# Optimization experiments

Measured on AMD Instinct MI355X. Metric: run time of the kernel, lower is better.

The kernel has to match this reference:

```python
import jax, jax.numpy as jnp
import numpy as np

D, H_DIM, HEADS = 512, 2048, 8

def rmsnorm(x, w):
    eps = jnp.finfo(x.dtype).eps
    return x * jax.lax.rsqrt(jnp.mean(x * x, axis=-1, keepdims=True) + eps) * w

def setup_inputs() -> dict:
    key = jax.random.key(0)
    ks = jax.random.split(key, 16)
    B, N = 2, 2048
    s_d = 1.0 / np.sqrt(D)
    s_h = 1.0 / np.sqrt(H_DIM)
    inp = {
        "x": jax.random.normal(ks[0], (B, N, D), jnp.float32),
        "DA": jax.random.randint(ks[1], (B, 1, N, N), 0, 2, jnp.int32),
        "Wq": jax.random.normal(ks[2], (D, D), jnp.float32) * s_d,
        "bq": jnp.zeros((D,), jnp.float32),
        "Wk": jax.random.normal(ks[3], (D, D), jnp.float32) * s_d,
        "bk": jnp.zeros((D,), jnp.float32),
        "Wv": jax.random.normal(ks[4], (D, D), jnp.float32) * s_d,
        "bv": jnp.zeros((D,), jnp.float32),
        "W1": jax.random.normal(ks[5], (H_DIM, D), jnp.float32) * s_d,
        "b1": jnp.zeros((H_DIM,), jnp.float32),
        "W2": jax.random.normal(ks[6], (H_DIM, D), jnp.float32) * s_d,
        "b2": jnp.zeros((H_DIM,), jnp.float32),
        "W3": jax.random.normal(ks[7], (D, H_DIM), jnp.float32) * s_h,
        "b3": jnp.zeros((D,), jnp.float32),
        "g1": jnp.ones((D,), jnp.float32),
        "g2": jnp.ones((D,), jnp.float32),
    }
    return inp

def reference(x, DA, Wq, bq, Wk, bk, Wv, bv, W1, b1, W2, b2, W3, b3, g1, g2):
    B, N, _ = x.shape
    hd = D // HEADS  # head_dim = 64
    xn = rmsnorm(x, g1)
    # projections (torch Linear: y = x @ W.T + b), split heads -> [B,H,N,hd]
    def split(t):
        return t.reshape(B, N, HEADS, hd).transpose(0, 2, 1, 3)
    q = split(xn @ Wq.T + bq)
    k = split(xn @ Wk.T + bk)
    v = split(xn @ Wv.T + bv)
    scores = jnp.einsum("bhnd,bhmd->bhnm", q, k) / np.sqrt(hd)
    scores = jnp.where(DA == 0, jnp.asarray(-1e20, scores.dtype), scores)
    attn = jax.nn.softmax(scores, axis=-1)
    o = jnp.einsum("bhnm,bhmd->bhnd", attn, v)
    o = o.transpose(0, 2, 1, 3).reshape(B, N, D)
    h = x + o
    hn = rmsnorm(h, g2)
    x2 = hn @ W1.T + b1
    x3 = hn @ W2.T + b2
    out = h + (jax.nn.silu(x2) * x3) @ W3.T + b3
    return out
```

## Files before the change

kernel.cpp:

```cpp
#include <hip/hip_runtime.h>

typedef unsigned short u16;
typedef unsigned int   u32;
typedef unsigned long long u64;

using bf16x8 = __attribute__((ext_vector_type(8))) __bf16;
using f32x4  = __attribute__((ext_vector_type(4))) float;
using us8    = __attribute__((ext_vector_type(8))) u16;
using us4v   = __attribute__((ext_vector_type(4))) u16;

#define NB_TOK   4096
#define DD       512
#define HDIM     2048
#define SEQ      2048
#define EPS_F32  1.1920929e-7f
#define SM_SHIFT2 23.083120654223414f
#define Q_SCALE   0.18033688011112042f

__device__ __forceinline__ u16 f32_to_bf16(float f) {
  u32 u = __float_as_uint(f);
  u += 0x7fffu + ((u >> 16) & 1u);
  return (u16)(u >> 16);
}
__device__ __forceinline__ float bf16_to_f32(u16 h) {
  return __uint_as_float(((u32)h) << 16);
}
__device__ __forceinline__ bf16x8 ld_frag(const u16* p) {
  return __builtin_bit_cast(bf16x8, *(const us8*)p);
}
__device__ __forceinline__ void gload_lds16(const void* g, void* l) {
  __builtin_amdgcn_global_load_lds(
      (__attribute__((address_space(1))) void*)(void*)g,
      (__attribute__((address_space(3))) void*)l, 16, 0, 0);
}

__global__ __launch_bounds__(256) void k_pre(
    const float* __restrict__ wq, const float* __restrict__ wk,
    const float* __restrict__ wv, const float* __restrict__ w1,
    const float* __restrict__ w2, const float* __restrict__ w3,
    const int* __restrict__ da, const float* __restrict__ x,
    const float* __restrict__ g1,
    u16* __restrict__ wqkv, u16* __restrict__ w1b,
    u16* __restrict__ w2b, u16* __restrict__ w3b,
    u64* __restrict__ maskT, u16* __restrict__ xn) {
  int bx = blockIdx.x;
  if (bx < 3840) {
    int e = (bx * 256 + threadIdx.x) * 4;
    const float* src; u16* dst; int off;
    if      (e <  262144) { src = wq; dst = wqkv;          off = e; }
    else if (e <  524288) { src = wk; dst = wqkv + 262144; off = e -  262144; }
    else if (e <  786432) { src = wv; dst = wqkv + 524288; off = e -  524288; }
    else if (e < 1835008) { src = w1; dst = w1b;           off = e -  786432; }
    else if (e < 2883584) { src = w2; dst = w2b;           off = e - 1835008; }
    else                  { src = w3; dst = w3b;           off = e - 2883584; }
    float4 v = *(const float4*)(src + off);
    us4v o;
    o[0] = f32_to_bf16(v.x); o[1] = f32_to_bf16(v.y);
    o[2] = f32_to_bf16(v.z); o[3] = f32_to_bf16(v.w);
    *(us4v*)(dst + off) = o;
  } else if (bx < 4864) {
    int lane = threadIdx.x & 63, wave = threadIdx.x >> 6;
    int row = (bx - 3840) * 4 + wave;
    int b = row >> 11, r = row & 2047;
    const int* src = da + (size_t)row * SEQ;
    #pragma unroll 4
    for (int w = 0; w < 32; ++w) {
      int d = src[w * 64 + lane];
      u64 bal = __ballot(d != 0);
      if (lane == 0) maskT[((size_t)(b * 32 + w)) * SEQ + r] = bal;
    }
  } else {
    int lane = threadIdx.x & 63, wave = threadIdx.x >> 6;
    int row = (bx - 4864) * 4 + wave;
    size_t base = (size_t)row * DD + lane * 8;
    float4 a = *(const float4*)(x + base);
    float4 b = *(const float4*)(x + base + 4);
    float ss = a.x*a.x + a.y*a.y + a.z*a.z + a.w*a.w
             + b.x*b.x + b.y*b.y + b.z*b.z + b.w*b.w;
    #pragma unroll
    for (int m = 1; m < 64; m <<= 1) ss += __shfl_xor(ss, m);
    float sc = rsqrtf(ss * (1.0f / DD) + EPS_F32);
    float4 ga = *(const float4*)(g1 + lane * 8);
    float4 gb = *(const float4*)(g1 + lane * 8 + 4);
    us8 o;
    o[0] = f32_to_bf16(a.x * sc * ga.x); o[1] = f32_to_bf16(a.y * sc * ga.y);
    o[2] = f32_to_bf16(a.z * sc * ga.z); o[3] = f32_to_bf16(a.w * sc * ga.w);
    o[4] = f32_to_bf16(b.x * sc * gb.x); o[5] = f32_to_bf16(b.y * sc * gb.y);
    o[6] = f32_to_bf16(b.z * sc * gb.z); o[7] = f32_to_bf16(b.w * sc * gb.w);
    *(us8*)(xn + base) = o;
  }
}

template <int NB>
__device__ __forceinline__ void gemm32(const u16* __restrict__ A,
                                       const u16* __restrict__ B0,
                                       const u16* __restrict__ B1,
                                       int K, int mblk, int nblk,
                                       int kbeg, int iters,
                                       u16* lA, u16* lB,
                                       f32x4 (*acc)[4][2]) {
  const int lane = threadIdx.x & 63, wave = threadIdx.x >> 6;
  const int l15 = lane & 15, quad = lane >> 4;
  const int wmt = (wave >> 1) * 4, wnt = (wave & 1) * 2;
  constexpr int CPW = 2 + NB;

  auto stage = [&](int buf, int k0) {
    #pragma unroll
    for (int i = 0; i < CPW; ++i) {
      int id = wave * CPW + i;
      if (id < 8) {
        gload_lds16(A + (size_t)(mblk + id * 16 + l15) * K + k0 + quad * 8,
                    lA + buf * 4096 + id * 512);
      } else {
        int id2 = id - 8, bi = id2 >> 2, nt = id2 & 3;
        const u16* B = bi ? B1 : B0;
        gload_lds16(B + (size_t)(nblk + nt * 16 + l15) * K + k0 + quad * 8,
                    lB + bi * 4096 + buf * 2048 + nt * 512);
      }
    }
  };

  stage(0, kbeg);
  __syncthreads();
  for (int it = 0; it < iters; ++it) {
    if (it + 1 < iters) stage((it + 1) & 1, kbeg + (it + 1) * 32);
    int buf = it & 1;
    bf16x8 af[4];
    #pragma unroll
    for (int mt = 0; mt < 4; ++mt)
      af[mt] = ld_frag(lA + buf * 4096 + (wmt + mt) * 512 + lane * 8);
    #pragma unroll
    for (int bi = 0; bi < NB; ++bi)
      #pragma unroll
      for (int nt = 0; nt < 2; ++nt) {
        bf16x8 b = ld_frag(lB + bi * 4096 + buf * 2048 + (wnt + nt) * 512 + lane * 8);
        #pragma unroll
        for (int mt = 0; mt < 4; ++mt)
          acc[bi][mt][nt] = __builtin_amdgcn_mfma_f32_16x16x32_bf16(
              af[mt], b, acc[bi][mt][nt], 0, 0, 0);
      }
    __syncthreads();
  }
}

__global__ __launch_bounds__(256, 4) void k_qkv(const u16* __restrict__ xn,
                                                const u16* __restrict__ wqkv,
                                                const float* __restrict__ bq,
                                                const float* __restrict__ bk,
                                                const float* __restrict__ bv,
                                                u16* __restrict__ qb,
                                                u16* __restrict__ kb,
                                                u16* __restrict__ vt) {
  __shared__ u16 lA[8192], lB[4096];
  int z = blockIdx.z;
  const u16* Bp = wqkv + z * (DD * DD);
  const float* bias = (z == 0) ? bq : ((z == 1) ? bk : bv);
  float scale = (z == 0) ? Q_SCALE : 1.0f;
  int mblk = blockIdx.x * 128, nblk = blockIdx.y * 64;
  f32x4 acc[1][4][2];
  #pragma unroll
  for (int mt = 0; mt < 4; ++mt)
    #pragma unroll
    for (int nt = 0; nt < 2; ++nt) acc[0][mt][nt] = (f32x4)0.0f;
  gemm32<1>(xn, Bp, nullptr, DD, mblk, nblk, 0, 16, lA, lB, acc);
  int lane = threadIdx.x & 63, wave = threadIdx.x >> 6;
  int l15 = lane & 15, quad = lane >> 4;
  int wm = (wave >> 1) * 64, wn = (wave & 1) * 32;
  if (z < 2) {
    u16* out = z ? kb : qb;
    #pragma unroll
    for (int mt = 0; mt < 4; ++mt)
      #pragma unroll
      for (int nt = 0; nt < 2; ++nt) {
        int n = nblk + wn + nt * 16 + l15;
        float bn = bias[n];
        #pragma unroll
        for (int r = 0; r < 4; ++r) {
          int m = mblk + wm + mt * 16 + quad * 4 + r;
          out[(size_t)m * DD + n] = f32_to_bf16((acc[0][mt][nt][r] + bn) * scale);
        }
      }
  } else {
    #pragma unroll
    for (int mt = 0; mt < 4; ++mt)
      #pragma unroll
      for (int nt = 0; nt < 2; ++nt) {
        int n = nblk + wn + nt * 16 + l15;
        float bn = bias[n];
        int m = mblk + wm + mt * 16 + quad * 4;
        int b = m >> 11, tok = m & 2047;
        us4v o;
        #pragma unroll
        for (int r = 0; r < 4; ++r) o[r] = f32_to_bf16(acc[0][mt][nt][r] + bn);
        *(us4v*)(vt + ((size_t)(b * 8 + (n >> 6)) * 64 + (n & 63)) * SEQ + tok) = o;
      }
  }
}

__global__ __launch_bounds__(256) void k_attn(const u16* __restrict__ q,
                                              const u16* __restrict__ k,
                                              const u16* __restrict__ vT,
                                              const u64* __restrict__ maskT,
                                              u16* __restrict__ Opart,
                                              float* __restrict__ lpart) {
  __shared__ u16 lK[8192], lV[8192], lP[4 * 32 * 72];
  int tid = threadIdx.x, lane = tid & 63, wave = tid >> 6;
  int l15 = lane & 15, quad = lane >> 4;
  int bh = blockIdx.y, b = bh >> 3, h = bh & 7;
  int q0 = blockIdx.x * 128;
  int z = blockIdx.z;
  int kvbase = z * 512;
  const u16* kg = k + (size_t)(b * SEQ + kvbase) * DD + h * 64;
  const u16* vg = vT + (size_t)bh * 64 * SEQ + kvbase;
  const u64* mg = maskT + ((size_t)(b * 32 + z * 8)) * SEQ + q0 + wave * 32 + l15;

  #pragma unroll
  for (int i = 0; i < 2; ++i) {
    int c = wave * 2 + i;
    int mt = c >> 1, ks = c & 1;
    gload_lds16(kg + (size_t)(mt * 16 + l15) * DD + ks * 32 + quad * 8, lK + c * 512);
    gload_lds16(vg + (size_t)(mt * 16 + l15) * SEQ + ks * 32 + quad * 8, lV + c * 512);
  }

  const u16* qrow = q + (size_t)(b * SEQ + q0 + wave * 32 + l15) * DD + h * 64;
  bf16x8 qa[2][2];
  #pragma unroll
  for (int nq = 0; nq < 2; ++nq)
    #pragma unroll
    for (int ks = 0; ks < 2; ++ks)
      qa[nq][ks] = ld_frag(qrow + (size_t)nq * 16 * DD + ks * 32 + quad * 8);
  __syncthreads();

  us8 ones_u;
  #pragma unroll
  for (int j = 0; j < 8; ++j) ones_u[j] = 0x3f80;
  const bf16x8 ones = __builtin_bit_cast(bf16x8, ones_u);

  f32x4 oa[2][4], oal[2];
  #pragma unroll
  for (int mq = 0; mq < 2; ++mq) {
    oal[mq] = (f32x4)0.0f;
    #pragma unroll
    for (int dt = 0; dt < 4; ++dt) oa[mq][dt] = (f32x4)0.0f;
  }

  u16* pw = lP + wave * 2304;

  for (int t = 0; t < 8; ++t) {
    const u16* lKc = lK + (t & 1) * 4096;
    const u16* lVc = lV + (t & 1) * 4096;

    u64 mw[2];
    #pragma unroll
    for (int nq = 0; nq < 2; ++nq)
      mw[nq] = mg[(size_t)t * SEQ + nq * 16] >> (quad * 4);

    if (t + 1 < 8) {
      int kv1 = (t + 1) * 64;
      u16* dK = lK + ((t + 1) & 1) * 4096;
      u16* dV = lV + ((t + 1) & 1) * 4096;
      #pragma unroll
      for (int i = 0; i < 2; ++i) {
        int c = wave * 2 + i;
        int mt = c >> 1, ks = c & 1;
        gload_lds16(kg + (size_t)(kv1 + mt * 16 + l15) * DD + ks * 32 + quad * 8, dK + c * 512);
        gload_lds16(vg + (size_t)(mt * 16 + l15) * SEQ + kv1 + ks * 32 + quad * 8, dV + c * 512);
      }
    }

    f32x4 sa[2][4];
    #pragma unroll
    for (int nq = 0; nq < 2; ++nq)
      #pragma unroll
      for (int mt = 0; mt < 4; ++mt) sa[nq][mt] = (f32x4)0.0f;
    #pragma unroll
    for (int ks = 0; ks < 2; ++ks) {
      bf16x8 ka[4];
      #pragma unroll
      for (int mt = 0; mt < 4; ++mt)
        ka[mt] = ld_frag(lKc + mt * 1024 + ks * 512 + lane * 8);
      #pragma unroll
      for (int nq = 0; nq < 2; ++nq)
        #pragma unroll
        for (int mt = 0; mt < 4; ++mt)
          sa[nq][mt] = __builtin_amdgcn_mfma_f32_16x16x32_bf16(
              ka[mt], qa[nq][ks], sa[nq][mt], 0, 0, 0);
    }

    #pragma unroll
    for (int nq = 0; nq < 2; ++nq)
      #pragma unroll
      for (int mt = 0; mt < 4; ++mt) {
        u32 nib = (u32)(mw[nq] >> (mt * 16)) & 0xFu;
        u32 pb[4];
        #pragma unroll
        for (int r = 0; r < 4; ++r) {
          float p = __builtin_amdgcn_exp2f(sa[nq][mt][r] - SM_SHIFT2);
          p = (nib >> r) & 1u ? p : 0.0f;
          pb[r] = __float_as_uint(p);
        }
        u32 lo = __builtin_amdgcn_perm(pb[1], pb[0], 0x07060302u);
        u32 hi = __builtin_amdgcn_perm(pb[3], pb[2], 0x07060302u);
        u64 pk = ((u64)hi << 32) | lo;
        *(u64*)(pw + (nq * 16 + l15) * 72 + mt * 16 + quad * 4) = pk;
      }

    #pragma unroll
    for (int ks = 0; ks < 2; ++ks) {
      bf16x8 pa[2], vb[4];
      #pragma unroll
      for (int mq = 0; mq < 2; ++mq)
        pa[mq] = ld_frag(pw + (mq * 16 + l15) * 72 + ks * 32 + quad * 8);
      #pragma unroll
      for (int dt = 0; dt < 4; ++dt)
        vb[dt] = ld_frag(lVc + dt * 1024 + ks * 512 + lane * 8);
      #pragma unroll
      for (int mq = 0; mq < 2; ++mq) {
        #pragma unroll
        for (int dt = 0; dt < 4; ++dt)
          oa[mq][dt] = __builtin_amdgcn_mfma_f32_16x16x32_bf16(
              pa[mq], vb[dt], oa[mq][dt], 0, 0, 0);
        oal[mq] = __builtin_amdgcn_mfma_f32_16x16x32_bf16(
            pa[mq], ones, oal[mq], 0, 0, 0);
      }
    }

    __syncthreads();
  }

  if (l15 == 0) {
    #pragma unroll
    for (int mq = 0; mq < 2; ++mq)
      #pragma unroll
      for (int r = 0; r < 4; ++r)
        lpart[((size_t)z * 16 + bh) * SEQ + q0 + wave * 32 + mq * 16 + quad * 4 + r] =
            oal[mq][r];
  }

  u16* Og = Opart + (size_t)z * NB_TOK * DD;
  #pragma unroll
  for (int mq = 0; mq < 2; ++mq)
    #pragma unroll
    for (int r = 0; r < 4; ++r) {
      int m = q0 + wave * 32 + mq * 16 + quad * 4 + r;
      u16* dst = Og + (size_t)(b * SEQ + m) * DD + h * 64;
      #pragma unroll
      for (int dt = 0; dt < 4; ++dt)
        dst[dt * 16 + l15] = f32_to_bf16(oa[mq][dt][r]);
    }
}

__global__ __launch_bounds__(256) void k_rms2(const float* __restrict__ x,
                                              const u16* __restrict__ Opart,
                                              const float* __restrict__ lpart,
                                              const float* __restrict__ b3,
                                              const float* __restrict__ g2,
                                              float* __restrict__ outinit,
                                              u16* __restrict__ hn) {
  int lane = threadIdx.x & 63, wave = threadIdx.x >> 6;
  int row = blockIdx.x * 4 + wave;
  int b = row >> 11, tok = row & 2047, hh = lane >> 3;
  size_t base = (size_t)row * DD + lane * 8;
  float lsum = 0.0f;
  #pragma unroll
  for (int z = 0; z < 4; ++z)
    lsum += lpart[((size_t)(z * 16 + b * 8 + hh)) * SEQ + tok];
  float inv = (lsum > 0.0f) ? (1.0f / lsum) : 0.0f;
  float ov[8] = {0,0,0,0,0,0,0,0};
  #pragma unroll
  for (int z = 0; z < 4; ++z) {
    us8 o = *(const us8*)(Opart + (size_t)z * NB_TOK * DD + base);
    #pragma unroll
    for (int j = 0; j < 8; ++j) ov[j] += bf16_to_f32(o[j]);
  }
  float4 a = *(const float4*)(x + base);
  float4 bb = *(const float4*)(x + base + 4);
  float hv[8];
  hv[0] = a.x  + ov[0] * inv; hv[1] = a.y  + ov[1] * inv;
  hv[2] = a.z  + ov[2] * inv; hv[3] = a.w  + ov[3] * inv;
  hv[4] = bb.x + ov[4] * inv; hv[5] = bb.y + ov[5] * inv;
  hv[6] = bb.z + ov[6] * inv; hv[7] = bb.w + ov[7] * inv;
  float ss = 0.0f;
  #pragma unroll
  for (int j = 0; j < 8; ++j) ss += hv[j] * hv[j];
  #pragma unroll
  for (int m = 1; m < 64; m <<= 1) ss += __shfl_xor(ss, m);
  float sc = rsqrtf(ss * (1.0f / DD) + EPS_F32);
  float4 c0 = *(const float4*)(b3 + lane * 8);
  float4 c1 = *(const float4*)(b3 + lane * 8 + 4);
  float4 w0 = {hv[0] + c0.x, hv[1] + c0.y, hv[2] + c0.z, hv[3] + c0.w};
  float4 w1 = {hv[4] + c1.x, hv[5] + c1.y, hv[6] + c1.z, hv[7] + c1.w};
  *(float4*)(outinit + base) = w0;
  *(float4*)(outinit + base + 4) = w1;
  float4 ga = *(const float4*)(g2 + lane * 8);
  float4 gb = *(const float4*)(g2 + lane * 8 + 4);
  us8 hb;
  hb[0] = f32_to_bf16(hv[0] * sc * ga.x); hb[1] = f32_to_bf16(hv[1] * sc * ga.y);
  hb[2] = f32_to_bf16(hv[2] * sc * ga.z); hb[3] = f32_to_bf16(hv[3] * sc * ga.w);
  hb[4] = f32_to_bf16(hv[4] * sc * gb.x); hb[5] = f32_to_bf16(hv[5] * sc * gb.y);
  hb[6] = f32_to_bf16(hv[6] * sc * gb.z); hb[7] = f32_to_bf16(hv[7] * sc * gb.w);
  *(us8*)(hn + base) = hb;
}

__global__ __launch_bounds__(256, 4) void k_ffn12(const u16* __restrict__ hn,
                                                  const u16* __restrict__ w1,
                                                  const u16* __restrict__ w2,
                                                  const float* __restrict__ b1,
                                                  const float* __restrict__ b2,
                                                  u16* __restrict__ g) {
  __shared__ u16 lA[8192], lB[8192];
  int mblk = blockIdx.x * 128, nblk = blockIdx.y * 64;
  f32x4 acc[2][4][2];
  #pragma unroll
  for (int bi = 0; bi < 2; ++bi)
    #pragma unroll
    for (int mt = 0; mt < 4; ++mt)
      #pragma unroll
      for (int nt = 0; nt < 2; ++nt) acc[bi][mt][nt] = (f32x4)0.0f;
  gemm32<2>(hn, w1, w2, DD, mblk, nblk, 0, 16, lA, lB, acc);
  int lane = threadIdx.x & 63, wave = threadIdx.x >> 6;
  int l15 = lane & 15, quad = lane >> 4;
  int wm = (wave >> 1) * 64, wn = (wave & 1) * 32;
  #pragma unroll
  for (int mt = 0; mt < 4; ++mt)
    #pragma unroll
    for (int nt = 0; nt < 2; ++nt) {
      int n = nblk + wn + nt * 16 + l15;
      float bb1 = b1[n], bb2 = b2[n];
      #pragma unroll
      for (int r = 0; r < 4; ++r) {
        int m = mblk + wm + mt * 16 + quad * 4 + r;
        float x2 = acc[0][mt][nt][r] + bb1;
        float x3 = acc[1][mt][nt][r] + bb2;
        float si = x2 / (1.0f + __expf(-x2));
        g[(size_t)m * HDIM + n] = f32_to_bf16(si * x3);
      }
    }
}

__global__ __launch_bounds__(256, 4) void k_ffn3(const u16* __restrict__ g,
                                                 const u16* __restrict__ w3,
                                                 float* __restrict__ out) {
  __shared__ u16 lA[8192], lB[4096];
  int mblk = blockIdx.x * 128, nblk = blockIdx.y * 64;
  f32x4 acc[1][4][2];
  #pragma unroll
  for (int mt = 0; mt < 4; ++mt)
    #pragma unroll
    for (int nt = 0; nt < 2; ++nt) acc[0][mt][nt] = (f32x4)0.0f;
  gemm32<1>(g, w3, nullptr, HDIM, mblk, nblk, 0, 64, lA, lB, acc);
  int lane = threadIdx.x & 63, wave = threadIdx.x >> 6;
  int l15 = lane & 15, quad = lane >> 4;
  int wm = (wave >> 1) * 64, wn = (wave & 1) * 32;
  #pragma unroll
  for (int mt = 0; mt < 4; ++mt)
    #pragma unroll
    for (int nt = 0; nt < 2; ++nt) {
      int n = nblk + wn + nt * 16 + l15;
      #pragma unroll
      for (int r = 0; r < 4; ++r) {
        int m = mblk + wm + mt * 16 + quad * 4 + r;
        size_t idx = (size_t)m * DD + n;
        out[idx] = out[idx] + acc[0][mt][nt][r];
      }
    }
}

#define MB(x) ((size_t)(x) * 1048576)
#define WS_XN    MB(0)
#define WS_WQKV  MB(4)
#define WS_W1B   MB(6)
#define WS_W2B   MB(8)
#define WS_W3B   MB(10)
#define WS_MASK  MB(12)
#define WS_QB    MB(16)
#define WS_KB    MB(20)
#define WS_VT    MB(24)
#define WS_OP    MB(28)
#define WS_LP    MB(44)
#define WS_HN    MB(45)
#define WS_G     MB(49)

extern "C" void kernel_launch(void* const* d_in, const int* in_sizes, int n_in,
                              void* d_out, int out_size, void* d_ws, size_t ws_size,
                              hipStream_t stream) {
  (void)in_sizes; (void)n_in; (void)out_size; (void)ws_size;
  const float* x  = (const float*)d_in[0];
  const int*   DA = (const int*)d_in[1];
  const float* Wq = (const float*)d_in[2];
  const float* bq = (const float*)d_in[3];
  const float* Wk = (const float*)d_in[4];
  const float* bk = (const float*)d_in[5];
  const float* Wv = (const float*)d_in[6];
  const float* bv = (const float*)d_in[7];
  const float* W1 = (const float*)d_in[8];
  const float* b1 = (const float*)d_in[9];
  const float* W2 = (const float*)d_in[10];
  const float* b2 = (const float*)d_in[11];
  const float* W3 = (const float*)d_in[12];
  const float* b3 = (const float*)d_in[13];
  const float* g1 = (const float*)d_in[14];
  const float* g2 = (const float*)d_in[15];
  float* out = (float*)d_out;
  char* w = (char*)d_ws;

  u16* xn   = (u16*)(w + WS_XN);
  u16* wqkv = (u16*)(w + WS_WQKV);
  u16* w1b  = (u16*)(w + WS_W1B);
  u16* w2b  = (u16*)(w + WS_W2B);
  u16* w3b  = (u16*)(w + WS_W3B);
  u64* mskT = (u64*)(w + WS_MASK);
  u16* qb   = (u16*)(w + WS_QB);
  u16* kb   = (u16*)(w + WS_KB);
  u16* vt   = (u16*)(w + WS_VT);
  u16* Op   = (u16*)(w + WS_OP);
  float* lp = (float*)(w + WS_LP);
  u16* hn   = (u16*)(w + WS_HN);
  u16* gb   = (u16*)(w + WS_G);

  k_pre<<<5888, 256, 0, stream>>>(Wq, Wk, Wv, W1, W2, W3, DA, x, g1,
                                  wqkv, w1b, w2b, w3b, mskT, xn);
  k_qkv<<<dim3(32, 8, 3), 256, 0, stream>>>(xn, wqkv, bq, bk, bv, qb, kb, vt);
  k_attn<<<dim3(16, 16, 4), 256, 0, stream>>>(qb, kb, vt, mskT, Op, lp);
  k_rms2<<<1024, 256, 0, stream>>>(x, Op, lp, b3, g2, out, hn);
  k_ffn12<<<dim3(32, 32), 256, 0, stream>>>(hn, w1b, w2b, b1, b2, gb);
  k_ffn3<<<dim3(32, 8), 256, 0, stream>>>(gb, w3b, out);
}
```

Before: 272.9 us.

## Pass attention probabilities via ds_bpermute instead of LDS round-trip; prefetch mask

Removes the per-wave LDS staging buffer for the softmax probability tile. The packed bf16 probabilities are instead rearranged from the QK^T accumulator layout into the PV MFMA operand layout with ds_bpermute shuffles in registers. It also prefetches the next tile's mask words one iteration ahead and sets a minimum-occupancy launch bound. The aim is to cut LDS writes/reads and the latency of the mask load, at the cost of extra bpermute instructions, selects and register pressure.

```diff
diff --git a/kernel.cpp b/kernel.cpp
--- a/kernel.cpp
+++ b/kernel.cpp
@@ -8,6 +8,7 @@
 using f32x4  = __attribute__((ext_vector_type(4))) float;
 using us8    = __attribute__((ext_vector_type(8))) u16;
 using us4v   = __attribute__((ext_vector_type(4))) u16;
+using u32x4  = __attribute__((ext_vector_type(4))) u32;
 
 #define NB_TOK   4096
 #define DD       512
@@ -197,13 +198,13 @@
   }
 }
 
-__global__ __launch_bounds__(256) void k_attn(const u16* __restrict__ q,
-                                              const u16* __restrict__ k,
-                                              const u16* __restrict__ vT,
-                                              const u64* __restrict__ maskT,
-                                              u16* __restrict__ Opart,
-                                              float* __restrict__ lpart) {
-  __shared__ u16 lK[8192], lV[8192], lP[4 * 32 * 72];
+__global__ __launch_bounds__(256, 4) void k_attn(const u16* __restrict__ q,
+                                                 const u16* __restrict__ k,
+                                                 const u16* __restrict__ vT,
+                                                 const u64* __restrict__ maskT,
+                                                 u16* __restrict__ Opart,
+                                                 float* __restrict__ lpart) {
+  __shared__ u16 lK[8192], lV[8192];
   int tid = threadIdx.x, lane = tid & 63, wave = tid >> 6;
   int l15 = lane & 15, quad = lane >> 4;
   int bh = blockIdx.y, b = bh >> 3, h = bh & 7;
@@ -236,6 +237,10 @@
   for (int j = 0; j < 8; ++j) ones_u[j] = 0x3f80;
   const bf16x8 ones = __builtin_bit_cast(bf16x8, ones_u);
 
+  const int idxA = (l15 + ((lane & 16) << 1)) * 4;
+  const int idxB = idxA + 64;
+  const bool hiTile = (quad & 2) != 0;
+
   f32x4 oa[2][4], oal[2];
   #pragma unroll
   for (int mq = 0; mq < 2; ++mq) {
@@ -244,18 +249,16 @@
     for (int dt = 0; dt < 4; ++dt) oa[mq][dt] = (f32x4)0.0f;
   }
 
-  u16* pw = lP + wave * 2304;
+  u64 mw[2] = { mg[0], mg[16] };
 
   for (int t = 0; t < 8; ++t) {
     const u16* lKc = lK + (t & 1) * 4096;
     const u16* lVc = lV + (t & 1) * 4096;
 
-    u64 mw[2];
-    #pragma unroll
-    for (int nq = 0; nq < 2; ++nq)
-      mw[nq] = mg[(size_t)t * SEQ + nq * 16] >> (quad * 4);
-
+    u64 mwn[2] = {0, 0};
     if (t + 1 < 8) {
+      mwn[0] = mg[(size_t)(t + 1) * SEQ];
+      mwn[1] = mg[(size_t)(t + 1) * SEQ + 16];
       int kv1 = (t + 1) * 64;
       u16* dK = lK + ((t + 1) & 1) * 4096;
       u16* dV = lV + ((t + 1) & 1) * 4096;
@@ -287,11 +290,13 @@
               ka[mt], qa[nq][ks], sa[nq][mt], 0, 0, 0);
     }
 
-    #pragma unroll
-    for (int nq = 0; nq < 2; ++nq)
+    u32 pk[2][4][2];
+    #pragma unroll
+    for (int nq = 0; nq < 2; ++nq) {
+      u64 mq64 = mw[nq] >> (quad * 4);
       #pragma unroll
       for (int mt = 0; mt < 4; ++mt) {
-        u32 nib = (u32)(mw[nq] >> (mt * 16)) & 0xFu;
+        u32 nib = (u32)(mq64 >> (mt * 16)) & 0xFu;
         u32 pb[4];
         #pragma unroll
         for (int r = 0; r < 4; ++r) {
@@ -299,32 +304,39 @@
           p = (nib >> r) & 1u ? p : 0.0f;
           pb[r] = __float_as_uint(p);
         }
-        u32 lo = __builtin_amdgcn_perm(pb[1], pb[0], 0x07060302u);
-        u32 hi = __builtin_amdgcn_perm(pb[3], pb[2], 0x07060302u);
-        u64 pk = ((u64)hi << 32) | lo;
-        *(u64*)(pw + (nq * 16 + l15) * 72 + mt * 16 + quad * 4) = pk;
-      }
+        pk[nq][mt][0] = __builtin_amdgcn_perm(pb[1], pb[0], 0x07060302u);
+        pk[nq][mt][1] = __builtin_amdgcn_perm(pb[3], pb[2], 0x07060302u);
+      }
+    }
 
     #pragma unroll
     for (int ks = 0; ks < 2; ++ks) {
-      bf16x8 pa[2], vb[4];
-      #pragma unroll
-      for (int mq = 0; mq < 2; ++mq)
-        pa[mq] = ld_frag(pw + (mq * 16 + l15) * 72 + ks * 32 + quad * 8);
+      bf16x8 vb[4];
       #pragma unroll
       for (int dt = 0; dt < 4; ++dt)
         vb[dt] = ld_frag(lVc + dt * 1024 + ks * 512 + lane * 8);
       #pragma unroll
       for (int mq = 0; mq < 2; ++mq) {
+        u32x4 regv;
+        #pragma unroll
+        for (int jr = 0; jr < 4; ++jr) {
+          int idx = (jr < 2) ? idxA : idxB;
+          int sel = jr & 1;
+          u32 va = (u32)__builtin_amdgcn_ds_bpermute(idx, (int)pk[mq][2 * ks][sel]);
+          u32 vbv = (u32)__builtin_amdgcn_ds_bpermute(idx, (int)pk[mq][2 * ks + 1][sel]);
+          regv[jr] = hiTile ? vbv : va;
+        }
+        bf16x8 pa = __builtin_bit_cast(bf16x8, regv);
         #pragma unroll
         for (int dt = 0; dt < 4; ++dt)
           oa[mq][dt] = __builtin_amdgcn_mfma_f32_16x16x32_bf16(
-              pa[mq], vb[dt], oa[mq][dt], 0, 0, 0);
+              pa, vb[dt], oa[mq][dt], 0, 0, 0);
         oal[mq] = __builtin_amdgcn_mfma_f32_16x16x32_bf16(
-            pa[mq], ones, oal[mq], 0, 0, 0);
-      }
-    }
-
+            pa, ones, oal[mq], 0, 0, 0);
+      }
+    }
+
+    mw[0] = mwn[0]; mw[1] = mwn[1];
     __syncthreads();
   }
 
```

Result: no change. 274.4 us (+0.5%).
